# Kernel tuning notes

Measured on AMD Instinct MI355X. Metric: run time of the kernel, lower is better.

The kernel has to match this reference:

```python
import jax, jax.numpy as jnp
import numpy as np

N_M, N_H = 50000, 50000
E = 600000
D_IN, D_OUT = 128, 128
LN_EPS = 1e-5
NORM_EPS = 1e-12


def _segment_mean(x, seg, n):
    # PyG 'mean' aggregation: sum / count, 0 for isolated nodes (count clamped to 1)
    s = jax.ops.segment_sum(x, seg, num_segments=n)
    c = jax.ops.segment_sum(jnp.ones((seg.shape[0], 1), x.dtype), seg, num_segments=n)
    return s / jnp.maximum(c, 1.0)


def _sage(t_src, t_dst, ei, Wl, bl, Wr):
    # SAGEConv: lin_l(mean_j x_j) + lin_r(x_i), then L2-normalize rows
    agg = _segment_mean(t_src[ei[0]], ei[1], t_dst.shape[0])
    out = agg @ Wl + bl + t_dst @ Wr
    nrm = jnp.maximum(jnp.linalg.norm(out, axis=-1, keepdims=True), NORM_EPS)
    return out / nrm


def _layer_norm(x, g, b):
    mu = jnp.mean(x, axis=-1, keepdims=True)
    v = jnp.var(x, axis=-1, keepdims=True)
    return (x - mu) / jnp.sqrt(v + LN_EPS) * g + b


def setup_inputs() -> dict:
    key = jax.random.key(0)
    ks = jax.random.split(key, 24)
    r = lambda i, shape: jax.random.normal(ks[i], shape, dtype=jnp.float32) * 0.05
    inp = {
        'x_microbe': jax.random.normal(ks[0], (N_M, D_IN), dtype=jnp.float32),
        'x_host': jax.random.normal(ks[1], (N_H, D_IN), dtype=jnp.float32),
        # per-node-type linear transforms
        'W_nt_m': r(2, (D_IN, D_OUT)), 'b_nt_m': r(3, (D_OUT,)),
        'W_nt_h': r(4, (D_IN, D_OUT)), 'b_nt_h': r(5, (D_OUT,)),
        # SAGEConv params per edge type (lin_l has bias, lin_r has no bias)
        'Wl_mm': r(6, (D_OUT, D_OUT)), 'bl_mm': r(7, (D_OUT,)), 'Wr_mm': r(8, (D_OUT, D_OUT)),
        'Wl_mh': r(9, (D_OUT, D_OUT)), 'bl_mh': r(10, (D_OUT,)), 'Wr_mh': r(11, (D_OUT, D_OUT)),
        'Wl_hm': r(12, (D_OUT, D_OUT)), 'bl_hm': r(13, (D_OUT,)), 'Wr_hm': r(14, (D_OUT, D_OUT)),
        # LayerNorm affine params per node type
        'g_m': jnp.ones((D_OUT,), jnp.float32), 'be_m': jnp.zeros((D_OUT,), jnp.float32),
        'g_h': jnp.ones((D_OUT,), jnp.float32), 'be_h': jnp.zeros((D_OUT,), jnp.float32),
        # edge indices [2, E]: row0 = src, row1 = dst
        'ei_mm': jax.random.randint(ks[15], (2, E), 0, N_M, dtype=jnp.int32),
        'ei_mh': jnp.stack([jax.random.randint(ks[16], (E,), 0, N_M, dtype=jnp.int32),
                            jax.random.randint(ks[17], (E,), 0, N_H, dtype=jnp.int32)]),
        'ei_hm': jnp.stack([jax.random.randint(ks[18], (E,), 0, N_H, dtype=jnp.int32),
                            jax.random.randint(ks[19], (E,), 0, N_M, dtype=jnp.int32)]),
    }
    return inp


def reference(x_microbe, x_host, W_nt_m, b_nt_m, W_nt_h, b_nt_h,
              Wl_mm, bl_mm, Wr_mm, Wl_mh, bl_mh, Wr_mh, Wl_hm, bl_hm, Wr_hm,
              g_m, be_m, g_h, be_h, ei_mm, ei_mh, ei_hm):
    # per-type linear transforms
    t_m = x_microbe @ W_nt_m + b_nt_m
    t_h = x_host @ W_nt_h + b_nt_h
    # SAGEConv per edge type
    o_mm = _sage(t_m, t_m, ei_mm, Wl_mm, bl_mm, Wr_mm)  # microbe -> microbe
    o_mh = _sage(t_m, t_h, ei_mh, Wl_mh, bl_mh, Wr_mh)  # microbe -> host
    o_hm = _sage(t_h, t_m, ei_hm, Wl_hm, bl_hm, Wr_hm)  # host -> microbe
    # HeteroConv aggr='mean' over edge types per dst node type
    conv_m = 0.5 * (o_mm + o_hm)
    conv_h = o_mh
    # residual + LayerNorm (dropout is identity in eval mode)
    out_m = _layer_norm(t_m + conv_m, g_m, be_m)
    out_h = _layer_norm(t_h + conv_h, g_h, be_h)
    return out_m, out_h
```

## Files before the change

kernel.cpp:

```cpp
#include <hip/hip_runtime.h>

typedef unsigned short u16;
typedef unsigned int u32;
typedef __attribute__((ext_vector_type(8))) short bf16x8;
typedef __attribute__((ext_vector_type(4))) float f32x4;

#define LDSN 13312
#define CHUNK 24576

__device__ __forceinline__ float bf_lo(u32 u){ return __uint_as_float(u << 16); }
__device__ __forceinline__ float bf_hi(u32 u){ return __uint_as_float(u & 0xffff0000u); }
__device__ __forceinline__ float bf2f(u16 v){ return __uint_as_float((u32)v << 16); }
__device__ __forceinline__ u16 f2bf(float f){
    u32 u = __float_as_uint(f);
    u32 r = (u + 0x7fffu + ((u >> 16) & 1u)) >> 16;
    return (u16)r;
}
__device__ __forceinline__ u32 pack2(float a, float b){
    return (u32)f2bf(a) | ((u32)f2bf(b) << 16);
}

__global__ __launch_bounds__(256) void prep_kernel(
    const int* __restrict__ d0, const int* __restrict__ d1, const int* __restrict__ d2,
    int E0, int E1, int E2, int n0, int n1, int n2,
    int c0, int c1, int c2, int R0, int R1, int R2,
    u16* __restrict__ C0, u16* __restrict__ C1, u16* __restrict__ C2, int HB2,
    const float* __restrict__ Wf0, const float* __restrict__ Wf1,
    const float* __restrict__ Wf2, const float* __restrict__ Wf3,
    const float* __restrict__ Wf4, const float* __restrict__ Wf5,
    u16* __restrict__ WF,
    const float* __restrict__ Xm, const float* __restrict__ Wm,
    const float* __restrict__ bm, u16* __restrict__ Tm, int NM,
    const float* __restrict__ Xh, const float* __restrict__ Wh,
    const float* __restrict__ bh, u16* __restrict__ Th, int NH,
    int gm, int gh)
{
    __shared__ u32 lc[LDSN];
    int bid = blockIdx.x;
    if (bid < HB2){
        const int* dp; int E, n, cc, rr; u16* cp;
        if (bid < c0 * R0){ dp = d0; E = E0; n = n0; cp = C0; cc = bid / R0; rr = bid % R0; }
        else if (bid < c0 * R0 + c1 * R1){ int l = bid - c0 * R0; dp = d1; E = E1; n = n1; cp = C1; cc = l / R1; rr = l % R1; }
        else { int l = bid - c0 * R0 - c1 * R1; dp = d2; E = E2; n = n2; cp = C2; cc = l / R2; rr = l % R2; }
        for (int i = threadIdx.x; i < LDSN; i += 256) lc[i] = 0;
        __syncthreads();
        int r0 = rr * LDSN, r1 = min(r0 + LDSN, n);
        int i0 = cc * CHUNK, i1 = min(i0 + CHUNK, E);
        for (int i = i0 + threadIdx.x; i < i1; i += 256){
            int x = dp[i];
            if ((unsigned)x < (unsigned)n && x >= r0 && x < r1)
                atomicAdd(&lc[x - r0], 1u);
        }
        __syncthreads();
        u16* op = cp + (size_t)cc * n;
        for (int x = r0 + threadIdx.x; x < r1; x += 256) op[x] = (u16)lc[x - r0];
        return;
    }
    bid -= HB2;
    if (bid < 6){
        const float* W = bid == 0 ? Wf0 : bid == 1 ? Wf1 : bid == 2 ? Wf2 :
                         bid == 3 ? Wf3 : bid == 4 ? Wf4 : Wf5;
        u16* dst = WF + (size_t)bid * 16384;
        #pragma unroll 4
        for (int k = 0; k < 64; ++k){
            int i = k * 256 + threadIdx.x;
            int j   = i & 7;
            int l16 = (i >> 3) & 15;
            int qd  = (i >> 7) & 3;
            int q   = (i >> 9) & 3;
            int tt  = (i >> 11) & 1;
            int w   = (i >> 12) & 3;
            dst[i] = f2bf(W[(q * 32 + qd * 8 + j) * 128 + (w * 32 + tt * 16 + l16)]);
        }
        return;
    }
    bid -= 6;
    const float *A, *W, *bias; u16* C; int N, lgrid, lbid;
    if (bid < gm){ A = Xm; W = Wm; bias = bm; C = Tm; N = NM; lgrid = gm; lbid = bid; }
    else         { A = Xh; W = Wh; bias = bh; C = Th; N = NH; lgrid = gh; lbid = bid - gm; }

    int tid = threadIdx.x;
    int wave = tid >> 6, lane = tid & 63;
    int colHalf = wave & 1;
    int ln16 = lane & 15, quad = lane >> 4;

    bf16x8 Bfrag[4][4];
    #pragma unroll
    for (int t = 0; t < 4; ++t){
        int col = colHalf * 64 + t * 16 + ln16;
        #pragma unroll
        for (int q = 0; q < 4; ++q){
            bf16x8 f;
            #pragma unroll
            for (int j = 0; j < 8; ++j)
                f[j] = (short)f2bf(W[(q * 32 + quad * 8 + j) * 128 + col]);
            Bfrag[t][q] = f;
        }
    }
    float bv[4];
    #pragma unroll
    for (int t = 0; t < 4; ++t)
        bv[t] = bias[colHalf * 64 + t * 16 + ln16];

    int rowBlocks = (N + 15) >> 4;
    for (int rb = lbid * 2 + (wave >> 1); rb < rowBlocks; rb += lgrid * 2){
        int row0 = rb * 16;
        int ar = row0 + ln16; if (ar > N - 1) ar = N - 1;
        const float* Arow = A + (size_t)ar * 128 + quad * 8;
        bf16x8 Af[4];
        #pragma unroll
        for (int q = 0; q < 4; ++q){
            f32x4 lo = *(const f32x4*)(Arow + q * 32);
            f32x4 hi = *(const f32x4*)(Arow + q * 32 + 4);
            bf16x8 f;
            #pragma unroll
            for (int j = 0; j < 4; ++j){ f[j] = (short)f2bf(lo[j]); f[4+j] = (short)f2bf(hi[j]); }
            Af[q] = f;
        }
        f32x4 acc[4];
        #pragma unroll
        for (int t = 0; t < 4; ++t) acc[t] = (f32x4){bv[t], bv[t], bv[t], bv[t]};
        #pragma unroll
        for (int q = 0; q < 4; ++q)
            #pragma unroll
            for (int t = 0; t < 4; ++t)
                acc[t] = __builtin_amdgcn_mfma_f32_16x16x32_bf16(Af[q], Bfrag[t][q], acc[t], 0, 0, 0);
        #pragma unroll
        for (int t = 0; t < 4; ++t){
            int col = colHalf * 64 + t * 16 + ln16;
            #pragma unroll
            for (int r = 0; r < 4; ++r){
                int row = row0 + quad * 4 + r;
                if (row < N) C[(size_t)row * 128 + col] = f2bf(acc[t][r]);
            }
        }
    }
}

__global__ __launch_bounds__(256) void scan_blocks_kernel(
    const u16* __restrict__ C0, const u16* __restrict__ C1, const u16* __restrict__ C2,
    int c0, int c1, int c2, int NM, int NH, int n,
    int* __restrict__ off, int* __restrict__ part)
{
    __shared__ int lds[256];
    int tid = threadIdx.x;
    int base = blockIdx.x * 2048 + tid * 8;
    int v[8]; int s = 0;
    #pragma unroll
    for (int j = 0; j < 8; ++j){
        int idx = base + j;
        int tot = 0;
        if (idx < n){
            const u16* cp; int ch, w, x;
            if (idx < NM){ cp = C0; ch = c0; w = NM; x = idx; }
            else if (idx < 2 * NM){ cp = C1; ch = c1; w = NM; x = idx - NM; }
            else { cp = C2; ch = c2; w = NH; x = idx - 2 * NM; }
            for (int cc = 0; cc < ch; ++cc) tot += cp[(size_t)cc * w + x];
        }
        v[j] = s; s += tot;
    }
    lds[tid] = s;
    __syncthreads();
    for (int d = 1; d < 256; d <<= 1){
        int t = (tid >= d) ? lds[tid - d] : 0;
        __syncthreads();
        lds[tid] += t;
        __syncthreads();
    }
    int thrBase = (tid > 0) ? lds[tid - 1] : 0;
    if (tid == 255) part[blockIdx.x] = lds[255];
    #pragma unroll
    for (int j = 0; j < 8; ++j){
        int idx = base + j;
        if (idx < n) off[idx] = thrBase + v[j];
    }
}

__global__ __launch_bounds__(128) void scan_part_kernel(
    int* __restrict__ part, int np, int* __restrict__ total_slot)
{
    __shared__ int lds[128];
    int tid = threadIdx.x;
    lds[tid] = (tid < np) ? part[tid] : 0;
    __syncthreads();
    for (int d = 1; d < 128; d <<= 1){
        int t = (tid >= d) ? lds[tid - d] : 0;
        __syncthreads();
        lds[tid] += t;
        __syncthreads();
    }
    if (tid < np) part[tid] = (tid > 0) ? lds[tid - 1] : 0;
    if (tid == 0) *total_slot = lds[np - 1 < 0 ? 0 : np - 1];
}

__global__ __launch_bounds__(256) void scan_add_kernel(
    int* __restrict__ off, const int* __restrict__ part, int n)
{
    int i = blockIdx.x * 256 + threadIdx.x;
    if (i < n) off[i] += part[i >> 11];
}

__global__ __launch_bounds__(256) void colbase_kernel(
    const u16* __restrict__ C0, const u16* __restrict__ C1, const u16* __restrict__ C2,
    int* __restrict__ B0, int* __restrict__ B1, int* __restrict__ B2,
    int c0, int c1, int c2, int NM, int NH, int n,
    const int* __restrict__ off)
{
    int idx = blockIdx.x * 256 + threadIdx.x;
    if (idx >= n) return;
    const u16* cp; int* bp; int ch, w, x;
    if (idx < NM){ cp = C0; bp = B0; ch = c0; w = NM; x = idx; }
    else if (idx < 2 * NM){ cp = C1; bp = B1; ch = c1; w = NM; x = idx - NM; }
    else { cp = C2; bp = B2; ch = c2; w = NH; x = idx - 2 * NM; }
    int run = off[idx];
    for (int cc = 0; cc < ch; ++cc){
        bp[(size_t)cc * w + x] = run;
        run += cp[(size_t)cc * w + x];
    }
}

__global__ __launch_bounds__(256) void fillL_kernel(
    const int* __restrict__ s0, const int* __restrict__ s1, const int* __restrict__ s2,
    const int* __restrict__ d0, const int* __restrict__ d1, const int* __restrict__ d2,
    int E0, int E1, int E2, int n0, int n1, int n2,
    int c0, int c1, int c2, int R0, int R1, int R2,
    const int* __restrict__ B0, const int* __restrict__ B1, const int* __restrict__ B2,
    int* __restrict__ slot)
{
    __shared__ u32 lc[LDSN];
    int bid = blockIdx.x;
    const int *dp, *sp, *bp; int E, n, cc, rr;
    if (bid < c0 * R0){ sp = s0; dp = d0; E = E0; n = n0; bp = B0; cc = bid / R0; rr = bid % R0; }
    else if (bid < c0 * R0 + c1 * R1){ int l = bid - c0 * R0; sp = s1; dp = d1; E = E1; n = n1; bp = B1; cc = l / R1; rr = l % R1; }
    else { int l = bid - c0 * R0 - c1 * R1; sp = s2; dp = d2; E = E2; n = n2; bp = B2; cc = l / R2; rr = l % R2; }
    for (int i = threadIdx.x; i < LDSN; i += 256) lc[i] = 0;
    __syncthreads();
    int r0 = rr * LDSN, r1 = min(r0 + LDSN, n);
    const int* bpc = bp + (size_t)cc * n;
    int i0 = cc * CHUNK, i1 = min(i0 + CHUNK, E);
    for (int i = i0 + threadIdx.x; i < i1; i += 256){
        int x = dp[i];
        if ((unsigned)x < (unsigned)n && x >= r0 && x < r1){
            u32 lr = atomicAdd(&lc[x - r0], 1u);
            slot[bpc[x] + (int)lr] = sp[i];
        }
    }
}

__global__ __launch_bounds__(256) void gather3_kernel(
    const u16* __restrict__ TM, const u16* __restrict__ TH,
    const int* __restrict__ off, const int* __restrict__ slot,
    u32* __restrict__ AGGM, u32* __restrict__ AGGH, int NM, int NH)
{
    int n3 = 2 * NM + NH;
    int wid = (int)((blockIdx.x * 256u + threadIdx.x) >> 6);
    int lane = threadIdx.x & 63;
    int nw = (gridDim.x * 256) >> 6;

    for (int id = wid; id < n3; id += nw){
        int b = off[id], e = off[id + 1];
        int deg = e - b;
        const u16* Tsrc; int nsrc;
        if (id < NM){ Tsrc = TM; nsrc = NM; }
        else if (id < 2 * NM){ Tsrc = TH; nsrc = NH; }
        else { Tsrc = TM; nsrc = NM; }

        int take = deg < 64 ? deg : 64;
        int ms = 0;
        if (lane < take){
            ms = slot[b + lane];
            if ((unsigned)ms >= (unsigned)nsrc) ms = 0;
        }

        float a0=0.f,a1=0.f,b0f=0.f,b1f=0.f,c0=0.f,c1=0.f,d0f=0.f,d1f=0.f;
        float e0=0.f,e1=0.f,f0=0.f,f1=0.f,g0=0.f,g1=0.f,h0=0.f,h1=0.f;
        int j = 0;
        for (; j + 8 <= take; j += 8){
            int i0 = __shfl(ms, j);     int i1 = __shfl(ms, j + 1);
            int i2 = __shfl(ms, j + 2); int i3 = __shfl(ms, j + 3);
            int i4 = __shfl(ms, j + 4); int i5 = __shfl(ms, j + 5);
            int i6 = __shfl(ms, j + 6); int i7 = __shfl(ms, j + 7);
            u32 u0 = *(const u32*)(Tsrc + (size_t)i0 * 128 + lane * 2);
            u32 u1 = *(const u32*)(Tsrc + (size_t)i1 * 128 + lane * 2);
            u32 u2 = *(const u32*)(Tsrc + (size_t)i2 * 128 + lane * 2);
            u32 u3 = *(const u32*)(Tsrc + (size_t)i3 * 128 + lane * 2);
            u32 u4 = *(const u32*)(Tsrc + (size_t)i4 * 128 + lane * 2);
            u32 u5 = *(const u32*)(Tsrc + (size_t)i5 * 128 + lane * 2);
            u32 u6 = *(const u32*)(Tsrc + (size_t)i6 * 128 + lane * 2);
            u32 u7 = *(const u32*)(Tsrc + (size_t)i7 * 128 + lane * 2);
            a0 += bf_lo(u0); a1 += bf_hi(u0);
            b0f += bf_lo(u1); b1f += bf_hi(u1);
            c0 += bf_lo(u2); c1 += bf_hi(u2);
            d0f += bf_lo(u3); d1f += bf_hi(u3);
            e0 += bf_lo(u4); e1 += bf_hi(u4);
            f0 += bf_lo(u5); f1 += bf_hi(u5);
            g0 += bf_lo(u6); g1 += bf_hi(u6);
            h0 += bf_lo(u7); h1 += bf_hi(u7);
        }
        for (; j + 4 <= take; j += 4){
            int i0 = __shfl(ms, j);     int i1 = __shfl(ms, j + 1);
            int i2 = __shfl(ms, j + 2); int i3 = __shfl(ms, j + 3);
            u32 u0 = *(const u32*)(Tsrc + (size_t)i0 * 128 + lane * 2);
            u32 u1 = *(const u32*)(Tsrc + (size_t)i1 * 128 + lane * 2);
            u32 u2 = *(const u32*)(Tsrc + (size_t)i2 * 128 + lane * 2);
            u32 u3 = *(const u32*)(Tsrc + (size_t)i3 * 128 + lane * 2);
            a0 += bf_lo(u0); a1 += bf_hi(u0);
            b0f += bf_lo(u1); b1f += bf_hi(u1);
            c0 += bf_lo(u2); c1 += bf_hi(u2);
            d0f += bf_lo(u3); d1f += bf_hi(u3);
        }
        for (; j < take; ++j){
            int i0 = __shfl(ms, j);
            u32 u0 = *(const u32*)(Tsrc + (size_t)i0 * 128 + lane * 2);
            a0 += bf_lo(u0); a1 += bf_hi(u0);
        }
        for (int j2 = b + 64; j2 < e; ++j2){
            int i0 = slot[j2];
            if ((unsigned)i0 >= (unsigned)nsrc) i0 = 0;
            u32 u0 = *(const u32*)(Tsrc + (size_t)i0 * 128 + lane * 2);
            a0 += bf_lo(u0); a1 += bf_hi(u0);
        }
        float s0 = ((a0 + b0f) + (c0 + d0f)) + ((e0 + f0) + (g0 + h0));
        float s1 = ((a1 + b1f) + (c1 + d1f)) + ((e1 + f1) + (g1 + h1));
        float inv = 1.0f / (float)(deg < 1 ? 1 : deg);
        u32 pv = pack2(s0 * inv, s1 * inv);
        if (id < 2 * NM) AGGM[(size_t)id * 64 + lane] = pv;
        else             AGGH[(size_t)(id - 2 * NM) * 64 + lane] = pv;
    }
}

template<int NT>
__global__ __launch_bounds__(256) void gemmln_kernel(
    const u32* __restrict__ AG1, const u32* __restrict__ AG2,
    const u16* __restrict__ Tdst,
    const u16* __restrict__ WFl1, const u16* __restrict__ WFr1, const float* __restrict__ bl1,
    const u16* __restrict__ WFl2, const u16* __restrict__ WFr2, const float* __restrict__ bl2,
    const float* __restrict__ g, const float* __restrict__ be,
    float* __restrict__ outp, int N, float scale)
{
    __shared__ float redN[NT][4][16];
    __shared__ float redS[2][4][16];

    int tid = threadIdx.x;
    int wave = tid >> 6, lane = tid & 63;
    int ln16 = lane & 15, quad = lane >> 4;

    const u32* AG[2] = {AG1, AG2};
    const u16* WFl[2] = {WFl1, WFl2};
    const u16* WFr[2] = {WFr1, WFr2};
    const float* bls[2] = {bl1, bl2};

    bf16x8 BL[NT][2][4], BR[NT][2][4];
    float bv[NT][2];
    #pragma unroll
    for (int et = 0; et < NT; ++et){
        #pragma unroll
        for (int t = 0; t < 2; ++t){
            bv[et][t] = bls[et][wave * 32 + t * 16 + ln16];
            #pragma unroll
            for (int q = 0; q < 4; ++q){
                int fo = ((((wave * 2 + t) * 4 + q) * 4 + quad) * 16 + ln16) * 8;
                BL[et][t][q] = *(const bf16x8*)(WFl[et] + fo);
                BR[et][t][q] = *(const bf16x8*)(WFr[et] + fo);
            }
        }
    }
    float gv[2], bev[2];
    #pragma unroll
    for (int t = 0; t < 2; ++t){
        int col = wave * 32 + t * 16 + ln16;
        gv[t] = g[col]; bev[t] = be[col];
    }

    int tiles = (N + 15) >> 4;
    for (int tile = blockIdx.x; tile < tiles; tile += gridDim.x){
        int row0 = tile * 16;
        int ar = row0 + ln16; if (ar > N - 1) ar = N - 1;
        const u16* Ar2 = Tdst + (size_t)ar * 128 + quad * 8;

        f32x4 acc[NT][2];
        #pragma unroll
        for (int et = 0; et < NT; ++et)
            #pragma unroll
            for (int t = 0; t < 2; ++t)
                acc[et][t] = (f32x4){bv[et][t], bv[et][t], bv[et][t], bv[et][t]};

        #pragma unroll
        for (int q = 0; q < 4; ++q){
            bf16x8 afr = *(const bf16x8*)(Ar2 + q * 32);
            #pragma unroll
            for (int et = 0; et < NT; ++et){
                bf16x8 afl = *(const bf16x8*)(AG[et] + (size_t)ar * 64 + q * 16 + quad * 4);
                #pragma unroll
                for (int t = 0; t < 2; ++t){
                    acc[et][t] = __builtin_amdgcn_mfma_f32_16x16x32_bf16(afl, BL[et][t][q], acc[et][t], 0, 0, 0);
                    acc[et][t] = __builtin_amdgcn_mfma_f32_16x16x32_bf16(afr, BR[et][t][q], acc[et][t], 0, 0, 0);
                }
            }
        }

        #pragma unroll
        for (int et = 0; et < NT; ++et){
            #pragma unroll
            for (int r = 0; r < 4; ++r){
                float s = acc[et][0][r] * acc[et][0][r] + acc[et][1][r] * acc[et][1][r];
                #pragma unroll
                for (int m = 1; m < 16; m <<= 1) s += __shfl_xor(s, m);
                if (ln16 == 0) redN[et][wave][quad * 4 + r] = s;
            }
        }
        __syncthreads();

        float yv[2][4];
        float lsum[4], lsq[4];
        #pragma unroll
        for (int r = 0; r < 4; ++r){
            int r16 = quad * 4 + r;
            int row = row0 + r16;
            int crow = row < N ? row : N - 1;
            float sc[NT];
            #pragma unroll
            for (int et = 0; et < NT; ++et){
                float tot = redN[et][0][r16] + redN[et][1][r16] + redN[et][2][r16] + redN[et][3][r16];
                sc[et] = scale / fmaxf(sqrtf(tot), 1e-12f);
            }
            float s1v = 0.f, s2v = 0.f;
            #pragma unroll
            for (int t = 0; t < 2; ++t){
                int col = wave * 32 + t * 16 + ln16;
                float y = bf2f(Tdst[(size_t)crow * 128 + col]);
                #pragma unroll
                for (int et = 0; et < NT; ++et) y += acc[et][t][r] * sc[et];
                yv[t][r] = y;
                s1v += y; s2v += y * y;
            }
            #pragma unroll
            for (int m = 1; m < 16; m <<= 1){ s1v += __shfl_xor(s1v, m); s2v += __shfl_xor(s2v, m); }
            lsum[r] = s1v; lsq[r] = s2v;
        }
        if (ln16 == 0){
            #pragma unroll
            for (int r = 0; r < 4; ++r){
                redS[0][wave][quad * 4 + r] = lsum[r];
                redS[1][wave][quad * 4 + r] = lsq[r];
            }
        }
        __syncthreads();

        #pragma unroll
        for (int r = 0; r < 4; ++r){
            int r16 = quad * 4 + r;
            int row = row0 + r16;
            if (row >= N) continue;
            float S1 = redS[0][0][r16] + redS[0][1][r16] + redS[0][2][r16] + redS[0][3][r16];
            float S2 = redS[1][0][r16] + redS[1][1][r16] + redS[1][2][r16] + redS[1][3][r16];
            float mean = S1 * (1.0f / 128.0f);
            float var = S2 * (1.0f / 128.0f) - mean * mean;
            float rstd = rsqrtf(var + 1e-5f);
            #pragma unroll
            for (int t = 0; t < 2; ++t){
                int col = wave * 32 + t * 16 + ln16;
                outp[(size_t)row * 128 + col] = (yv[t][r] - mean) * rstd * gv[t] + bev[t];
            }
        }
        __syncthreads();
    }
}

extern "C" void kernel_launch(void* const* d_in, const int* in_sizes, int n_in,
                              void* d_out, int out_size, void* d_ws, size_t ws_size,
                              hipStream_t stream) {
    const float* xm    = (const float*)d_in[0];
    const float* xh    = (const float*)d_in[1];
    const float* Wnt_m = (const float*)d_in[2];  const float* bnt_m = (const float*)d_in[3];
    const float* Wnt_h = (const float*)d_in[4];  const float* bnt_h = (const float*)d_in[5];
    const float* Wl_mm = (const float*)d_in[6];  const float* bl_mm = (const float*)d_in[7];
    const float* Wr_mm = (const float*)d_in[8];
    const float* Wl_mh = (const float*)d_in[9];  const float* bl_mh = (const float*)d_in[10];
    const float* Wr_mh = (const float*)d_in[11];
    const float* Wl_hm = (const float*)d_in[12]; const float* bl_hm = (const float*)d_in[13];
    const float* Wr_hm = (const float*)d_in[14];
    const float* g_m   = (const float*)d_in[15]; const float* be_m  = (const float*)d_in[16];
    const float* g_h   = (const float*)d_in[17]; const float* be_h  = (const float*)d_in[18];
    const int* ei_mm = (const int*)d_in[19];
    const int* ei_mh = (const int*)d_in[20];
    const int* ei_hm = (const int*)d_in[21];

    const int D = 128;
    const int NM = in_sizes[0] / D;
    const int NH = in_sizes[1] / D;
    const int E1 = in_sizes[19] / 2;
    const int E2 = in_sizes[20] / 2;
    const int E3 = in_sizes[21] / 2;
    const int Esum = E1 + E2 + E3;
    const int n3 = 2 * NM + NH;

    const int c0 = (E1 + CHUNK - 1) / CHUNK;
    const int c1 = (E3 + CHUNK - 1) / CHUNK;
    const int c2 = (E2 + CHUNK - 1) / CHUNK;
    const int R0 = (NM + LDSN - 1) / LDSN;
    const int R1 = (NM + LDSN - 1) / LDSN;
    const int R2 = (NH + LDSN - 1) / LDSN;
    const int HB2 = c0 * R0 + c1 * R1 + c2 * R2;

    char* ws = (char*)d_ws;
    size_t woff = 0;
    auto alloc = [&](size_t bytes) -> void* {
        void* p = ws + woff;
        woff += (bytes + 255) & ~(size_t)255;
        return p;
    };
    u16* T_M   = (u16*)alloc((size_t)NM * D * 2);
    u16* T_H   = (u16*)alloc((size_t)NH * D * 2);
    u16* CNT16 = (u16*)alloc(((size_t)(c0 + c1) * NM + (size_t)c2 * NH) * 2);
    int* OFF3  = (int*)alloc((size_t)(n3 + 1) * 4);
    int* SLOT3 = (int*)alloc((size_t)Esum * 4);
    int* PART  = (int*)alloc(1024 * 4);
    u16* WF    = (u16*)alloc((size_t)6 * 16384 * 2);
    u32* AGGM  = (u32*)alloc((size_t)2 * NM * 64 * 4);
    if (woff > ws_size) return;

    u16* C0p = CNT16;
    u16* C1p = C0p + (size_t)c0 * NM;
    u16* C2p = C1p + (size_t)c1 * NM;

    int* B0p = (int*)d_out;
    int* B1p = B0p + (size_t)c0 * NM;
    int* B2p = B1p + (size_t)c1 * NM;
    u32* AGGH = (u32*)d_out;

    float* OUT_M = (float*)d_out;
    float* OUT_H = (float*)d_out + (size_t)NM * D;

    const int gm = 1024, gh = 1024;
    const int scanBlocks = (n3 + 2047) / 2048;

    prep_kernel<<<HB2 + 6 + gm + gh, 256, 0, stream>>>(
        ei_mm + E1, ei_hm + E3, ei_mh + E2,
        E1, E3, E2, NM, NM, NH,
        c0, c1, c2, R0, R1, R2,
        C0p, C1p, C2p, HB2,
        Wl_mm, Wr_mm, Wl_hm, Wr_hm, Wl_mh, Wr_mh, WF,
        xm, Wnt_m, bnt_m, T_M, NM,
        xh, Wnt_h, bnt_h, T_H, NH, gm, gh);

    scan_blocks_kernel<<<scanBlocks, 256, 0, stream>>>(
        C0p, C1p, C2p, c0, c1, c2, NM, NH, n3, OFF3, PART);
    scan_part_kernel<<<1, 128, 0, stream>>>(PART, scanBlocks, OFF3 + n3);
    scan_add_kernel<<<(n3 + 255) / 256, 256, 0, stream>>>(OFF3, PART, n3);
    colbase_kernel<<<(n3 + 255) / 256, 256, 0, stream>>>(
        C0p, C1p, C2p, B0p, B1p, B2p, c0, c1, c2, NM, NH, n3, OFF3);

    fillL_kernel<<<HB2, 256, 0, stream>>>(
        ei_mm, ei_hm, ei_mh,
        ei_mm + E1, ei_hm + E3, ei_mh + E2,
        E1, E3, E2, NM, NM, NH,
        c0, c1, c2, R0, R1, R2,
        B0p, B1p, B2p, SLOT3);

    gather3_kernel<<<2048, 256, 0, stream>>>(
        T_M, T_H, OFF3, SLOT3, AGGM, AGGH, NM, NH);

    gemmln_kernel<1><<<1024, 256, 0, stream>>>(
        AGGH, nullptr, T_H,
        WF + 4 * 16384, WF + 5 * 16384, bl_mh,
        nullptr, nullptr, nullptr,
        g_h, be_h, OUT_H, NH, 1.0f);
    gemmln_kernel<2><<<1024, 256, 0, stream>>>(
        AGGM, AGGM + (size_t)NM * 64, T_M,
        WF + 0 * 16384, WF + 1 * 16384, bl_mm,
        WF + 2 * 16384, WF + 3 * 16384, bl_hm,
        g_m, be_m, OUT_M, NM, 0.5f);
}
```

Before: 476.6 us.

## Record per-edge local ranks in histogram pass and fill CSR without re-histogramming

The histogram pass now moves into its own kernel and stores each edge's LDS atomic rank as a u16 in scratch space carved from the output buffer. The CSR fill becomes a flat per-edge scatter that uses the stored rank instead of re-running the LDS histogram over range-partitioned blocks, where each edge chunk was read once per row range. The scan-add step is folded into colbase, which removes one launch. The edge chunk size is reduced, which raises the number of column-base entries and histogram blocks. The cost is an extra u16 write and read per edge, and the histogram no longer overlaps with the prep work inside one launch.

```diff
diff --git a/kernel.cpp b/kernel.cpp
--- a/kernel.cpp
+++ b/kernel.cpp
@@ -6,7 +6,7 @@
 typedef __attribute__((ext_vector_type(4))) float f32x4;
 
 #define LDSN 13312
-#define CHUNK 24576
+#define CHUNK 16384
 
 __device__ __forceinline__ float bf_lo(u32 u){ return __uint_as_float(u << 16); }
 __device__ __forceinline__ float bf_hi(u32 u){ return __uint_as_float(u & 0xffff0000u); }
@@ -21,10 +21,6 @@
 }
 
 __global__ __launch_bounds__(256) void prep_kernel(
-    const int* __restrict__ d0, const int* __restrict__ d1, const int* __restrict__ d2,
-    int E0, int E1, int E2, int n0, int n1, int n2,
-    int c0, int c1, int c2, int R0, int R1, int R2,
-    u16* __restrict__ C0, u16* __restrict__ C1, u16* __restrict__ C2, int HB2,
     const float* __restrict__ Wf0, const float* __restrict__ Wf1,
     const float* __restrict__ Wf2, const float* __restrict__ Wf3,
     const float* __restrict__ Wf4, const float* __restrict__ Wf5,
@@ -35,28 +31,7 @@
     const float* __restrict__ bh, u16* __restrict__ Th, int NH,
     int gm, int gh)
 {
-    __shared__ u32 lc[LDSN];
     int bid = blockIdx.x;
-    if (bid < HB2){
-        const int* dp; int E, n, cc, rr; u16* cp;
-        if (bid < c0 * R0){ dp = d0; E = E0; n = n0; cp = C0; cc = bid / R0; rr = bid % R0; }
-        else if (bid < c0 * R0 + c1 * R1){ int l = bid - c0 * R0; dp = d1; E = E1; n = n1; cp = C1; cc = l / R1; rr = l % R1; }
-        else { int l = bid - c0 * R0 - c1 * R1; dp = d2; E = E2; n = n2; cp = C2; cc = l / R2; rr = l % R2; }
-        for (int i = threadIdx.x; i < LDSN; i += 256) lc[i] = 0;
-        __syncthreads();
-        int r0 = rr * LDSN, r1 = min(r0 + LDSN, n);
-        int i0 = cc * CHUNK, i1 = min(i0 + CHUNK, E);
-        for (int i = i0 + threadIdx.x; i < i1; i += 256){
-            int x = dp[i];
-            if ((unsigned)x < (unsigned)n && x >= r0 && x < r1)
-                atomicAdd(&lc[x - r0], 1u);
-        }
-        __syncthreads();
-        u16* op = cp + (size_t)cc * n;
-        for (int x = r0 + threadIdx.x; x < r1; x += 256) op[x] = (u16)lc[x - r0];
-        return;
-    }
-    bid -= HB2;
     if (bid < 6){
         const float* W = bid == 0 ? Wf0 : bid == 1 ? Wf1 : bid == 2 ? Wf2 :
                          bid == 3 ? Wf3 : bid == 4 ? Wf4 : Wf5;
@@ -137,6 +112,33 @@
     }
 }
 
+__global__ __launch_bounds__(256) void histL_kernel(
+    const int* __restrict__ d0, const int* __restrict__ d1, const int* __restrict__ d2,
+    u16* __restrict__ rk0, u16* __restrict__ rk1, u16* __restrict__ rk2,
+    int E0, int E1, int E2, int n0, int n1, int n2,
+    int c0, int c1, int c2, int R0, int R1, int R2,
+    u16* __restrict__ C0, u16* __restrict__ C1, u16* __restrict__ C2)
+{
+    __shared__ u32 lc[LDSN];
+    int bid = blockIdx.x;
+    const int* dp; u16 *rk, *cp; int E, n, cc, rr;
+    if (bid < c0 * R0){ dp = d0; rk = rk0; cp = C0; E = E0; n = n0; cc = bid / R0; rr = bid % R0; }
+    else if (bid < c0 * R0 + c1 * R1){ int l = bid - c0 * R0; dp = d1; rk = rk1; cp = C1; E = E1; n = n1; cc = l / R1; rr = l % R1; }
+    else { int l = bid - c0 * R0 - c1 * R1; dp = d2; rk = rk2; cp = C2; E = E2; n = n2; cc = l / R2; rr = l % R2; }
+    for (int i = threadIdx.x; i < LDSN; i += 256) lc[i] = 0;
+    __syncthreads();
+    int r0 = rr * LDSN, r1 = min(r0 + LDSN, n);
+    int i0 = cc * CHUNK, i1 = min(i0 + CHUNK, E);
+    for (int i = i0 + threadIdx.x; i < i1; i += 256){
+        int x = dp[i];
+        if ((unsigned)x < (unsigned)n && x >= r0 && x < r1)
+            rk[i] = (u16)atomicAdd(&lc[x - r0], 1u);
+    }
+    __syncthreads();
+    u16* op = cp + (size_t)cc * n;
+    for (int x = r0 + threadIdx.x; x < r1; x += 256) op[x] = (u16)lc[x - r0];
+}
+
 __global__ __launch_bounds__(256) void scan_blocks_kernel(
     const u16* __restrict__ C0, const u16* __restrict__ C1, const u16* __restrict__ C2,
     int c0, int c1, int c2, int NM, int NH, int n,
@@ -193,56 +195,51 @@
     if (tid == 0) *total_slot = lds[np - 1 < 0 ? 0 : np - 1];
 }
 
-__global__ __launch_bounds__(256) void scan_add_kernel(
-    int* __restrict__ off, const int* __restrict__ part, int n)
-{
-    int i = blockIdx.x * 256 + threadIdx.x;
-    if (i < n) off[i] += part[i >> 11];
-}
-
 __global__ __launch_bounds__(256) void colbase_kernel(
     const u16* __restrict__ C0, const u16* __restrict__ C1, const u16* __restrict__ C2,
     int* __restrict__ B0, int* __restrict__ B1, int* __restrict__ B2,
     int c0, int c1, int c2, int NM, int NH, int n,
-    const int* __restrict__ off)
+    int* __restrict__ off, const int* __restrict__ part)
 {
     int idx = blockIdx.x * 256 + threadIdx.x;
     if (idx >= n) return;
+    int run = off[idx] + part[idx >> 11];
+    off[idx] = run;
     const u16* cp; int* bp; int ch, w, x;
     if (idx < NM){ cp = C0; bp = B0; ch = c0; w = NM; x = idx; }
     else if (idx < 2 * NM){ cp = C1; bp = B1; ch = c1; w = NM; x = idx - NM; }
     else { cp = C2; bp = B2; ch = c2; w = NH; x = idx - 2 * NM; }
-    int run = off[idx];
     for (int cc = 0; cc < ch; ++cc){
         bp[(size_t)cc * w + x] = run;
         run += cp[(size_t)cc * w + x];
     }
 }
 
-__global__ __launch_bounds__(256) void fillL_kernel(
+__global__ __launch_bounds__(256) void fill3_kernel(
     const int* __restrict__ s0, const int* __restrict__ s1, const int* __restrict__ s2,
     const int* __restrict__ d0, const int* __restrict__ d1, const int* __restrict__ d2,
+    const u16* __restrict__ rk0, const u16* __restrict__ rk1, const u16* __restrict__ rk2,
     int E0, int E1, int E2, int n0, int n1, int n2,
-    int c0, int c1, int c2, int R0, int R1, int R2,
     const int* __restrict__ B0, const int* __restrict__ B1, const int* __restrict__ B2,
     int* __restrict__ slot)
 {
-    __shared__ u32 lc[LDSN];
-    int bid = blockIdx.x;
-    const int *dp, *sp, *bp; int E, n, cc, rr;
-    if (bid < c0 * R0){ sp = s0; dp = d0; E = E0; n = n0; bp = B0; cc = bid / R0; rr = bid % R0; }
-    else if (bid < c0 * R0 + c1 * R1){ int l = bid - c0 * R0; sp = s1; dp = d1; E = E1; n = n1; bp = B1; cc = l / R1; rr = l % R1; }
-    else { int l = bid - c0 * R0 - c1 * R1; sp = s2; dp = d2; E = E2; n = n2; bp = B2; cc = l / R2; rr = l % R2; }
-    for (int i = threadIdx.x; i < LDSN; i += 256) lc[i] = 0;
-    __syncthreads();
-    int r0 = rr * LDSN, r1 = min(r0 + LDSN, n);
-    const int* bpc = bp + (size_t)cc * n;
-    int i0 = cc * CHUNK, i1 = min(i0 + CHUNK, E);
-    for (int i = i0 + threadIdx.x; i < i1; i += 256){
-        int x = dp[i];
-        if ((unsigned)x < (unsigned)n && x >= r0 && x < r1){
-            u32 lr = atomicAdd(&lc[x - r0], 1u);
-            slot[bpc[x] + (int)lr] = sp[i];
+    int t = blockIdx.y;
+    const int* sp = t == 0 ? s0 : (t == 1 ? s1 : s2);
+    const int* dp = t == 0 ? d0 : (t == 1 ? d1 : d2);
+    const u16* rk = t == 0 ? rk0 : (t == 1 ? rk1 : rk2);
+    const int* bp = t == 0 ? B0 : (t == 1 ? B1 : B2);
+    int E = t == 0 ? E0 : (t == 1 ? E1 : E2);
+    int n = t == 0 ? n0 : (t == 1 ? n1 : n2);
+    int base = blockIdx.x * 1024 + threadIdx.x;
+    #pragma unroll
+    for (int k = 0; k < 4; ++k){
+        int i = base + k * 256;
+        if (i < E){
+            int x = dp[i];
+            if ((unsigned)x < (unsigned)n){
+                int cc = i / CHUNK;
+                slot[bp[(size_t)cc * n + x] + (int)rk[i]] = sp[i];
+            }
         }
     }
 }
@@ -527,6 +524,8 @@
     int* B0p = (int*)d_out;
     int* B1p = B0p + (size_t)c0 * NM;
     int* B2p = B1p + (size_t)c1 * NM;
+    u16* RK  = (u16*)(B2p + (size_t)c2 * NH);
+    u16* rk0 = RK, *rk1 = RK + E1, *rk2 = RK + E1 + E3;
     u32* AGGH = (u32*)d_out;
 
     float* OUT_M = (float*)d_out;
@@ -534,28 +533,32 @@
 
     const int gm = 1024, gh = 1024;
     const int scanBlocks = (n3 + 2047) / 2048;
-
-    prep_kernel<<<HB2 + 6 + gm + gh, 256, 0, stream>>>(
-        ei_mm + E1, ei_hm + E3, ei_mh + E2,
-        E1, E3, E2, NM, NM, NH,
-        c0, c1, c2, R0, R1, R2,
-        C0p, C1p, C2p, HB2,
+    int Emax = E1 > E2 ? E1 : E2; if (E3 > Emax) Emax = E3;
+    const dim3 egrid((Emax + 1023) / 1024, 3);
+
+    prep_kernel<<<6 + gm + gh, 256, 0, stream>>>(
         Wl_mm, Wr_mm, Wl_hm, Wr_hm, Wl_mh, Wr_mh, WF,
         xm, Wnt_m, bnt_m, T_M, NM,
         xh, Wnt_h, bnt_h, T_H, NH, gm, gh);
 
+    histL_kernel<<<HB2, 256, 0, stream>>>(
+        ei_mm + E1, ei_hm + E3, ei_mh + E2,
+        rk0, rk1, rk2,
+        E1, E3, E2, NM, NM, NH,
+        c0, c1, c2, R0, R1, R2,
+        C0p, C1p, C2p);
+
     scan_blocks_kernel<<<scanBlocks, 256, 0, stream>>>(
         C0p, C1p, C2p, c0, c1, c2, NM, NH, n3, OFF3, PART);
     scan_part_kernel<<<1, 128, 0, stream>>>(PART, scanBlocks, OFF3 + n3);
-    scan_add_kernel<<<(n3 + 255) / 256, 256, 0, stream>>>(OFF3, PART, n3);
     colbase_kernel<<<(n3 + 255) / 256, 256, 0, stream>>>(
-        C0p, C1p, C2p, B0p, B1p, B2p, c0, c1, c2, NM, NH, n3, OFF3);
-
-    fillL_kernel<<<HB2, 256, 0, stream>>>(
+        C0p, C1p, C2p, B0p, B1p, B2p, c0, c1, c2, NM, NH, n3, OFF3, PART);
+
+    fill3_kernel<<<egrid, 256, 0, stream>>>(
         ei_mm, ei_hm, ei_mh,
         ei_mm + E1, ei_hm + E3, ei_mh + E2,
+        rk0, rk1, rk2,
         E1, E3, E2, NM, NM, NH,
-        c0, c1, c2, R0, R1, R2,
         B0p, B1p, B2p, SLOT3);
 
     gather3_kernel<<<2048, 256, 0, stream>>>(
```

Result: no change. 473.3 us (-0.7%).
